# Kernel tuning notes

Hardware: AMD Instinct MI355X
Metric: run time of the kernel (lower is better)

Reference implementation:

```python
import jax, jax.numpy as jnp
import numpy as np


def setup_inputs() -> dict:
    key = jax.random.key(0)
    k1, k2 = jax.random.split(key)
    B, S, D, T = 64, 512, 768, 384
    hidden_states = jax.random.normal(k1, (B, S, D), dtype=jnp.float32)
    # sorted per-row segment ids: each subtoken belongs to a token index in [0, T)
    segment_ids = jnp.sort(jax.random.randint(k2, (B, S), 0, T), axis=-1)
    return {"hidden_states": hidden_states, "segment_ids": segment_ids, "num_tokens": T}


def reference(hidden_states, segment_ids, num_tokens):
    # Segment-mean of subtoken embeddings into token embeddings.
    # Equivalent to the original running-mean loop:
    #   prev + (next - prev) / n_subtoken_per_token  == mean over the group.
    B, S, D = hidden_states.shape
    # flatten batch into segment ids so one segment_sum handles all sequences
    flat_ids = (segment_ids + jnp.arange(B, dtype=segment_ids.dtype)[:, None] * num_tokens).reshape(-1)
    sums = jax.ops.segment_sum(hidden_states.reshape(-1, D), flat_ids,
                               num_segments=B * num_tokens)  # [B*T, D]
    counts = jax.ops.segment_sum(jnp.ones((B * S,), dtype=hidden_states.dtype), flat_ids,
                                 num_segments=B * num_tokens)  # [B*T]
    # tokens with no subtokens stay zero (original initializes with zeros)
    means = sums / jnp.maximum(counts, 1.0)[:, None]
    return means.reshape(B, num_tokens, D)
```

## Files before the change

kernel.cpp:

```cpp
#include <hip/hip_runtime.h>


#define PHASE2_WAVES 4

__global__ void bounds_pairs_kernel(const int* __restrict__ seg,
                                    const int* __restrict__ num_tokens_p,
                                    int2* __restrict__ pairs,
                                    int BS_total,
                                    int BT) {
  const int T = num_tokens_p[0];
  const int B = BT / T;
  const int S = BS_total / B;
  const int idx = blockIdx.x * blockDim.x + threadIdx.x;
  if (idx >= BS_total) return;
  const int b = idx / S;
  const int s = idx - b * S;
  const int cur = seg[idx];
  const int prev = (s == 0) ? -1 : seg[idx - 1];
  int2* __restrict__ prow = pairs + (size_t)b * T;

  for (int t = prev + 1; t <= cur; ++t) {
    prow[t].x = idx;
    if (t > 0) prow[t - 1].y = idx;
  }
  if (s == S - 1) {
    const int end = b * S + S;
    for (int t = cur + 1; t <= T; ++t) {
      if (t < T) prow[t].x = end;
      prow[t - 1].y = end;
    }
  }
}

__global__ void __launch_bounds__(64 * PHASE2_WAVES) seg_mean_d768(
    const float* __restrict__ hs,
    const int2*  __restrict__ pairs,
    float*       __restrict__ out,
    int BT) {
  const int wave = threadIdx.x >> 6;
  const int lane = threadIdx.x & 63;
  const int gstride = gridDim.x * PHASE2_WAVES;

  int g = blockIdx.x * PHASE2_WAVES + wave;
  if (g >= BT) return;
  int2 lh = pairs[g];

  while (true) {
    const int gn = g + gstride;
    int2 lh_next;
    if (gn < BT) lh_next = pairs[gn];

    const int cnt = lh.y - lh.x;
    const float4* __restrict__ p =
        (const float4*)hs + (size_t)lh.x * 192 + lane;

    float4 a0 = make_float4(0.f, 0.f, 0.f, 0.f);
    float4 a1 = a0, a2 = a0;
    for (int r = 0; r < cnt; ++r) {
      float4 v0 = p[0];
      float4 v1 = p[64];
      float4 v2 = p[128];
      a0.x += v0.x; a0.y += v0.y; a0.z += v0.z; a0.w += v0.w;
      a1.x += v1.x; a1.y += v1.y; a1.z += v1.z; a1.w += v1.w;
      a2.x += v2.x; a2.y += v2.y; a2.z += v2.z; a2.w += v2.w;
      p += 192;
    }

    const float inv = (cnt > 0) ? (1.0f / (float)cnt) : 0.0f;
    float4* __restrict__ q = (float4*)out + (size_t)g * 192 + lane;
    q[0]   = make_float4(a0.x * inv, a0.y * inv, a0.z * inv, a0.w * inv);
    q[64]  = make_float4(a1.x * inv, a1.y * inv, a1.z * inv, a1.w * inv);
    q[128] = make_float4(a2.x * inv, a2.y * inv, a2.z * inv, a2.w * inv);

    if (gn >= BT) break;
    g = gn;
    lh = lh_next;
  }
}

__global__ void __launch_bounds__(64 * PHASE2_WAVES) seg_mean_generic(
    const float* __restrict__ hs,
    const int2*  __restrict__ pairs,
    float*       __restrict__ out,
    int BT,
    int dv4) {
  const int wave = threadIdx.x >> 6;
  const int lane = threadIdx.x & 63;
  const int gstride = gridDim.x * PHASE2_WAVES;

  for (int g = blockIdx.x * PHASE2_WAVES + wave; g < BT; g += gstride) {
    const int2 lh = pairs[g];
    const int cnt = lh.y - lh.x;
    const float inv = (cnt > 0) ? (1.0f / (float)cnt) : 0.0f;

    for (int c = lane; c < dv4; c += 64) {
      const float4* __restrict__ p = (const float4*)hs + (size_t)lh.x * dv4 + c;
      float4 acc = make_float4(0.f, 0.f, 0.f, 0.f);
      for (int r = 0; r < cnt; ++r) {
        float4 v = *p;
        acc.x += v.x; acc.y += v.y; acc.z += v.z; acc.w += v.w;
        p += dv4;
      }
      ((float4*)(out + (size_t)g * (dv4 * 4)))[c] =
          make_float4(acc.x * inv, acc.y * inv, acc.z * inv, acc.w * inv);
    }
  }
}

__global__ void __launch_bounds__(192) seg_mean_search_kernel(
    const float* __restrict__ hs,
    const int* __restrict__ seg,
    const int* __restrict__ num_tokens_p,
    float* __restrict__ out,
    int BS_total,
    int D) {
  const int T = num_tokens_p[0];
  const int BT = gridDim.x;
  const int S = (int)(((long long)BS_total * T) / BT);
  const int b = blockIdx.x / T;
  const int t = blockIdx.x - b * T;
  const int* __restrict__ row = seg + (size_t)b * S;

  int lo = 0, n = S;
  while (n > 0) {
    int half = n >> 1;
    int mid = lo + half;
    if (row[mid] < t) { lo = mid + 1; n -= half + 1; } else { n = half; }
  }
  int hi = lo; n = S - lo;
  while (n > 0) {
    int half = n >> 1;
    int mid = hi + half;
    if (row[mid] < t + 1) { hi = mid + 1; n -= half + 1; } else { n = half; }
  }
  const int cnt = hi - lo;

  const int d4 = threadIdx.x;
  const int rowstride4 = D >> 2;
  const float4* __restrict__ p =
      (const float4*)(hs + ((size_t)b * S + lo) * D) + d4;

  float4 acc = make_float4(0.f, 0.f, 0.f, 0.f);
  for (int s = 0; s < cnt; ++s) {
    float4 v = p[(size_t)s * rowstride4];
    acc.x += v.x; acc.y += v.y; acc.z += v.z; acc.w += v.w;
  }
  const float inv = (cnt > 0) ? (1.0f / (float)cnt) : 0.0f;
  float4 o = make_float4(acc.x * inv, acc.y * inv, acc.z * inv, acc.w * inv);
  ((float4*)(out + (size_t)blockIdx.x * D))[d4] = o;
}

extern "C" void kernel_launch(void* const* d_in, const int* in_sizes, int n_in,
                              void* d_out, int out_size, void* d_ws, size_t ws_size,
                              hipStream_t stream) {
  const float* hs = (const float*)d_in[0];
  const int* seg = (const int*)d_in[1];
  const int* num_tokens_p = (const int*)d_in[2];
  float* out = (float*)d_out;

  const int BS_total = in_sizes[1];
  const int D = in_sizes[0] / in_sizes[1];
  const int BT = out_size / D;

  const size_t ws_needed = (size_t)8 * (size_t)BT;

  if (ws_size >= ws_needed) {
    int2* pairs = (int2*)d_ws;

    const int threads1 = 256;
    const int grid1 = (BS_total + threads1 - 1) / threads1;
    hipLaunchKernelGGL(bounds_pairs_kernel, dim3(grid1), dim3(threads1), 0, stream,
                       seg, num_tokens_p, pairs, BS_total, BT);

    const int maxBlocks = 2048;
    const int needBlocks = (BT + PHASE2_WAVES - 1) / PHASE2_WAVES;
    const int grid2 = (needBlocks < maxBlocks) ? needBlocks : maxBlocks;

    if (D == 768) {
      hipLaunchKernelGGL(seg_mean_d768, dim3(grid2), dim3(64 * PHASE2_WAVES), 0,
                         stream, hs, pairs, out, BT);
    } else {
      hipLaunchKernelGGL(seg_mean_generic, dim3(grid2), dim3(64 * PHASE2_WAVES), 0,
                         stream, hs, pairs, out, BT, D / 4);
    }
  } else {
    hipLaunchKernelGGL(seg_mean_search_kernel, dim3(BT), dim3(D / 4), 0, stream,
                       hs, seg, num_tokens_p, out, BS_total, D);
  }
}
```

Before: 178.0 us.

## Process spans of four tokens per wave with a 4-deep register load pipeline

The D=768 segment-mean kernel now gives each wave a contiguous span of four tokens and streams their subtoken rows through a software pipeline that keeps four rows of loads in flight in registers. Outputs are flushed each time a token boundary is crossed, and the grid is sized so there is no grid-stride loop. The aim is to hide memory latency, since each token has only about one or two rows and the old loop had few independent loads per wave. In exchange it uses more registers per thread, adds boundary-tracking branches, and launches more, smaller blocks.

```diff
diff --git a/kernel.cpp b/kernel.cpp
--- a/kernel.cpp
+++ b/kernel.cpp
@@ -1,7 +1,8 @@
 #include <hip/hip_runtime.h>
 
 
-#define PHASE2_WAVES 4
+#define SPAN_K 4
+#define WPB    4
 
 __global__ void bounds_pairs_kernel(const int* __restrict__ seg,
                                     const int* __restrict__ num_tokens_p,
@@ -32,53 +33,96 @@
   }
 }
 
-__global__ void __launch_bounds__(64 * PHASE2_WAVES) seg_mean_d768(
+__global__ void __launch_bounds__(64 * WPB, 4) seg_mean_span_d768(
     const float* __restrict__ hs,
     const int2*  __restrict__ pairs,
     float*       __restrict__ out,
     int BT) {
   const int wave = threadIdx.x >> 6;
   const int lane = threadIdx.x & 63;
-  const int gstride = gridDim.x * PHASE2_WAVES;
-
-  int g = blockIdx.x * PHASE2_WAVES + wave;
-  if (g >= BT) return;
-  int2 lh = pairs[g];
-
-  while (true) {
-    const int gn = g + gstride;
-    int2 lh_next;
-    if (gn < BT) lh_next = pairs[gn];
-
-    const int cnt = lh.y - lh.x;
-    const float4* __restrict__ p =
-        (const float4*)hs + (size_t)lh.x * 192 + lane;
-
-    float4 a0 = make_float4(0.f, 0.f, 0.f, 0.f);
-    float4 a1 = a0, a2 = a0;
-    for (int r = 0; r < cnt; ++r) {
-      float4 v0 = p[0];
-      float4 v1 = p[64];
-      float4 v2 = p[128];
-      a0.x += v0.x; a0.y += v0.y; a0.z += v0.z; a0.w += v0.w;
-      a1.x += v1.x; a1.y += v1.y; a1.z += v1.z; a1.w += v1.w;
-      a2.x += v2.x; a2.y += v2.y; a2.z += v2.z; a2.w += v2.w;
-      p += 192;
-    }
-
-    const float inv = (cnt > 0) ? (1.0f / (float)cnt) : 0.0f;
-    float4* __restrict__ q = (float4*)out + (size_t)g * 192 + lane;
-    q[0]   = make_float4(a0.x * inv, a0.y * inv, a0.z * inv, a0.w * inv);
-    q[64]  = make_float4(a1.x * inv, a1.y * inv, a1.z * inv, a1.w * inv);
-    q[128] = make_float4(a2.x * inv, a2.y * inv, a2.z * inv, a2.w * inv);
-
-    if (gn >= BT) break;
-    g = gn;
-    lh = lh_next;
-  }
-}
-
-__global__ void __launch_bounds__(64 * PHASE2_WAVES) seg_mean_generic(
+  const int g0 = (blockIdx.x * WPB + wave) * SPAN_K;
+  if (g0 >= BT) return;
+  const int nTok = (BT - g0 < SPAN_K) ? (BT - g0) : SPAN_K;
+
+  const int2 pL = pairs[g0 + nTok - 1];
+  const int sEnd = pL.y;
+  const int s0 = pairs[g0].x;
+  const int s1 = (nTok > 1) ? pairs[g0 + 1].x : sEnd;
+  const int s2 = (nTok > 2) ? pairs[g0 + 2].x : sEnd;
+  const int s3 = (nTok > 3) ? pairs[g0 + 3].x : sEnd;
+  const int s4 = sEnd;
+
+  const float4* __restrict__ hsv = (const float4*)hs;
+
+#define ISSUE(X0, X1, X2, ROW)                                   \
+  do {                                                           \
+    const float4* _p = hsv + (size_t)(ROW) * 192 + lane;         \
+    X0 = _p[0]; X1 = _p[64]; X2 = _p[128];                       \
+  } while (0)
+
+  float4 A0, A1, A2, B0, B1, B2, C0, C1, C2, D0, D1, D2;
+  int rowI = s0;
+  if (rowI < s4) { ISSUE(A0, A1, A2, rowI); ++rowI; }
+  if (rowI < s4) { ISSUE(B0, B1, B2, rowI); ++rowI; }
+  if (rowI < s4) { ISSUE(C0, C1, C2, rowI); ++rowI; }
+  if (rowI < s4) { ISSUE(D0, D1, D2, rowI); ++rowI; }
+
+  float4 acc0 = make_float4(0.f, 0.f, 0.f, 0.f);
+  float4 acc1 = acc0, acc2 = acc0;
+  int rowC = s0;
+  int tok = 0;
+  int curLo = s0;
+  int nb1 = s1, nb2 = s2, nb3 = s3;
+
+#define FLUSH()                                                               \
+  while (tok < nTok && rowC == nb1) {                                         \
+    const int _cnt = rowC - curLo;                                            \
+    const float _inv = (_cnt > 0) ? (1.0f / (float)_cnt) : 0.0f;              \
+    float4* _q = (float4*)out + (size_t)(g0 + tok) * 192 + lane;              \
+    _q[0]   = make_float4(acc0.x * _inv, acc0.y * _inv, acc0.z * _inv, acc0.w * _inv); \
+    _q[64]  = make_float4(acc1.x * _inv, acc1.y * _inv, acc1.z * _inv, acc1.w * _inv); \
+    _q[128] = make_float4(acc2.x * _inv, acc2.y * _inv, acc2.z * _inv, acc2.w * _inv); \
+    acc0 = make_float4(0.f, 0.f, 0.f, 0.f); acc1 = acc0; acc2 = acc0;         \
+    curLo = rowC; ++tok;                                                      \
+    nb1 = nb2; nb2 = nb3; nb3 = s4;                                           \
+  }
+
+#define CONSUME(X0, X1, X2)                                                   \
+  do {                                                                        \
+    acc0.x += X0.x; acc0.y += X0.y; acc0.z += X0.z; acc0.w += X0.w;           \
+    acc1.x += X1.x; acc1.y += X1.y; acc1.z += X1.z; acc1.w += X1.w;           \
+    acc2.x += X2.x; acc2.y += X2.y; acc2.z += X2.z; acc2.w += X2.w;           \
+    ++rowC;                                                                   \
+  } while (0)
+
+  FLUSH();
+  while (rowC < s4) {
+    CONSUME(A0, A1, A2);
+    if (rowI < s4) { ISSUE(A0, A1, A2, rowI); ++rowI; }
+    FLUSH();
+    if (rowC >= s4) break;
+
+    CONSUME(B0, B1, B2);
+    if (rowI < s4) { ISSUE(B0, B1, B2, rowI); ++rowI; }
+    FLUSH();
+    if (rowC >= s4) break;
+
+    CONSUME(C0, C1, C2);
+    if (rowI < s4) { ISSUE(C0, C1, C2, rowI); ++rowI; }
+    FLUSH();
+    if (rowC >= s4) break;
+
+    CONSUME(D0, D1, D2);
+    if (rowI < s4) { ISSUE(D0, D1, D2, rowI); ++rowI; }
+    FLUSH();
+  }
+
+#undef CONSUME
+#undef FLUSH
+#undef ISSUE
+}
+
+__global__ void __launch_bounds__(256) seg_mean_generic(
     const float* __restrict__ hs,
     const int2*  __restrict__ pairs,
     float*       __restrict__ out,
@@ -86,9 +130,9 @@
     int dv4) {
   const int wave = threadIdx.x >> 6;
   const int lane = threadIdx.x & 63;
-  const int gstride = gridDim.x * PHASE2_WAVES;
-
-  for (int g = blockIdx.x * PHASE2_WAVES + wave; g < BT; g += gstride) {
+  const int gstride = gridDim.x * 4;
+
+  for (int g = blockIdx.x * 4 + wave; g < BT; g += gstride) {
     const int2 lh = pairs[g];
     const int cnt = lh.y - lh.x;
     const float inv = (cnt > 0) ? (1.0f / (float)cnt) : 0.0f;
@@ -172,15 +216,15 @@
     hipLaunchKernelGGL(bounds_pairs_kernel, dim3(grid1), dim3(threads1), 0, stream,
                        seg, num_tokens_p, pairs, BS_total, BT);
 
-    const int maxBlocks = 2048;
-    const int needBlocks = (BT + PHASE2_WAVES - 1) / PHASE2_WAVES;
-    const int grid2 = (needBlocks < maxBlocks) ? needBlocks : maxBlocks;
-
     if (D == 768) {
-      hipLaunchKernelGGL(seg_mean_d768, dim3(grid2), dim3(64 * PHASE2_WAVES), 0,
+      const int tokensPerBlock = SPAN_K * WPB;
+      const int grid2 = (BT + tokensPerBlock - 1) / tokensPerBlock;
+      hipLaunchKernelGGL(seg_mean_span_d768, dim3(grid2), dim3(64 * WPB), 0,
                          stream, hs, pairs, out, BT);
     } else {
-      hipLaunchKernelGGL(seg_mean_generic, dim3(grid2), dim3(64 * PHASE2_WAVES), 0,
+      const int needBlocks = (BT + 3) / 4;
+      const int grid2 = (needBlocks < 2048) ? needBlocks : 2048;
+      hipLaunchKernelGGL(seg_mean_generic, dim3(grid2), dim3(256), 0,
                          stream, hs, pairs, out, BT, D / 4);
     }
   } else {
```

New measurement: 177.7 us. About the same (-0.1%).

## Use one 192-thread block per token with count specializations and nontemporal stores

Applied to the files above, without the earlier changes.

The D=768 path now launches one 192-thread block per output token instead of a grid-stride loop of one wave per token, so each thread handles one float4 column. Counts of 0, 1 and 2 get dedicated branches, and larger counts use a loop unrolled by two. Outputs are written with nontemporal stores to reduce cache pollution. This raises parallelism and memory-level concurrency at the cost of more blocks (24576) and dropping the prefetch of the next token's bounds.

```diff
diff --git a/kernel.cpp b/kernel.cpp
--- a/kernel.cpp
+++ b/kernel.cpp
@@ -1,7 +1,7 @@
 #include <hip/hip_runtime.h>
 
 
-#define PHASE2_WAVES 4
+typedef float f32x4_v __attribute__((ext_vector_type(4)));
 
 __global__ void bounds_pairs_kernel(const int* __restrict__ seg,
                                     const int* __restrict__ num_tokens_p,
@@ -32,53 +32,52 @@
   }
 }
 
-__global__ void __launch_bounds__(64 * PHASE2_WAVES) seg_mean_d768(
+__global__ void __launch_bounds__(192) seg_mean_tok_d768(
     const float* __restrict__ hs,
     const int2*  __restrict__ pairs,
-    float*       __restrict__ out,
-    int BT) {
-  const int wave = threadIdx.x >> 6;
-  const int lane = threadIdx.x & 63;
-  const int gstride = gridDim.x * PHASE2_WAVES;
+    float*       __restrict__ out) {
+  const int g = blockIdx.x;
+  const int2 lh = pairs[g];
+  const int cnt = lh.y - lh.x;
+  const int d4 = threadIdx.x;
 
-  int g = blockIdx.x * PHASE2_WAVES + wave;
-  if (g >= BT) return;
-  int2 lh = pairs[g];
+  const float4* __restrict__ p =
+      (const float4*)hs + (size_t)lh.x * 192 + d4;
+  f32x4_v* __restrict__ q = (f32x4_v*)out + (size_t)g * 192 + d4;
 
-  while (true) {
-    const int gn = g + gstride;
-    int2 lh_next;
-    if (gn < BT) lh_next = pairs[gn];
+  float4 o;
+  if (cnt == 1) {
+    o = p[0];
+  } else if (cnt == 0) {
+    o = make_float4(0.f, 0.f, 0.f, 0.f);
+  } else if (cnt == 2) {
+    float4 a = p[0];
+    float4 b = p[192];
+    o = make_float4((a.x + b.x) * 0.5f, (a.y + b.y) * 0.5f,
+                    (a.z + b.z) * 0.5f, (a.w + b.w) * 0.5f);
+  } else {
+    float4 acc = make_float4(0.f, 0.f, 0.f, 0.f);
+    int r = 0;
+    for (; r + 1 < cnt; r += 2) {
+      float4 a = p[(size_t)r * 192];
+      float4 b = p[(size_t)(r + 1) * 192];
+      acc.x += a.x + b.x; acc.y += a.y + b.y;
+      acc.z += a.z + b.z; acc.w += a.w + b.w;
+    }
+    if (r < cnt) {
+      float4 a = p[(size_t)r * 192];
+      acc.x += a.x; acc.y += a.y; acc.z += a.z; acc.w += a.w;
+    }
+    const float inv = 1.0f / (float)cnt;
+    o = make_float4(acc.x * inv, acc.y * inv, acc.z * inv, acc.w * inv);
+  }
 
-    const int cnt = lh.y - lh.x;
-    const float4* __restrict__ p =
-        (const float4*)hs + (size_t)lh.x * 192 + lane;
-
-    float4 a0 = make_float4(0.f, 0.f, 0.f, 0.f);
-    float4 a1 = a0, a2 = a0;
-    for (int r = 0; r < cnt; ++r) {
-      float4 v0 = p[0];
-      float4 v1 = p[64];
-      float4 v2 = p[128];
-      a0.x += v0.x; a0.y += v0.y; a0.z += v0.z; a0.w += v0.w;
-      a1.x += v1.x; a1.y += v1.y; a1.z += v1.z; a1.w += v1.w;
-      a2.x += v2.x; a2.y += v2.y; a2.z += v2.z; a2.w += v2.w;
-      p += 192;
-    }
-
-    const float inv = (cnt > 0) ? (1.0f / (float)cnt) : 0.0f;
-    float4* __restrict__ q = (float4*)out + (size_t)g * 192 + lane;
-    q[0]   = make_float4(a0.x * inv, a0.y * inv, a0.z * inv, a0.w * inv);
-    q[64]  = make_float4(a1.x * inv, a1.y * inv, a1.z * inv, a1.w * inv);
-    q[128] = make_float4(a2.x * inv, a2.y * inv, a2.z * inv, a2.w * inv);
-
-    if (gn >= BT) break;
-    g = gn;
-    lh = lh_next;
-  }
+  f32x4_v ov;
+  ov.x = o.x; ov.y = o.y; ov.z = o.z; ov.w = o.w;
+  __builtin_nontemporal_store(ov, q);
 }
 
-__global__ void __launch_bounds__(64 * PHASE2_WAVES) seg_mean_generic(
+__global__ void __launch_bounds__(256) seg_mean_generic(
     const float* __restrict__ hs,
     const int2*  __restrict__ pairs,
     float*       __restrict__ out,
@@ -86,9 +85,9 @@
     int dv4) {
   const int wave = threadIdx.x >> 6;
   const int lane = threadIdx.x & 63;
-  const int gstride = gridDim.x * PHASE2_WAVES;
+  const int gstride = gridDim.x * 4;
 
-  for (int g = blockIdx.x * PHASE2_WAVES + wave; g < BT; g += gstride) {
+  for (int g = blockIdx.x * 4 + wave; g < BT; g += gstride) {
     const int2 lh = pairs[g];
     const int cnt = lh.y - lh.x;
     const float inv = (cnt > 0) ? (1.0f / (float)cnt) : 0.0f;
@@ -172,15 +171,13 @@
     hipLaunchKernelGGL(bounds_pairs_kernel, dim3(grid1), dim3(threads1), 0, stream,
                        seg, num_tokens_p, pairs, BS_total, BT);
 
-    const int maxBlocks = 2048;
-    const int needBlocks = (BT + PHASE2_WAVES - 1) / PHASE2_WAVES;
-    const int grid2 = (needBlocks < maxBlocks) ? needBlocks : maxBlocks;
-
     if (D == 768) {
-      hipLaunchKernelGGL(seg_mean_d768, dim3(grid2), dim3(64 * PHASE2_WAVES), 0,
-                         stream, hs, pairs, out, BT);
+      hipLaunchKernelGGL(seg_mean_tok_d768, dim3(BT), dim3(192), 0, stream,
+                         hs, pairs, out);
     } else {
-      hipLaunchKernelGGL(seg_mean_generic, dim3(grid2), dim3(64 * PHASE2_WAVES), 0,
+      const int needBlocks = (BT + 3) / 4;
+      const int grid2 = (needBlocks < 2048) ? needBlocks : 2048;
+      hipLaunchKernelGGL(seg_mean_generic, dim3(grid2), dim3(256), 0,
                          stream, hs, pairs, out, BT, D / 4);
     }
   } else {
```

Measured after the change: 172.7 us. 1.03x faster.

## Split D768 segment mean into row-chunk blocks plus per-token fixup blocks

Applied to the files above, without the earlier changes.

Replaces the per-token grid-stride kernel with a hybrid launch. Chunk blocks each load 16 consecutive rows and emit means for segments that lie entirely inside the chunk. Fixup blocks, one wave per token, handle segments that cross a chunk boundary and empty tokens. The aim is to spread input reads evenly across many blocks with high memory-level parallelism, and outputs are written with nontemporal stores. The cost is a more complex boundary-detection scheme and a larger launch that now depends on the bounds workspace and the raw segment ids together.

```diff
diff --git a/kernel.cpp b/kernel.cpp
--- a/kernel.cpp
+++ b/kernel.cpp
@@ -1,7 +1,10 @@
 #include <hip/hip_runtime.h>
 
 
-#define PHASE2_WAVES 4
+typedef float f32x4_v __attribute__((ext_vector_type(4)));
+
+#define CHUNK 16
+#define CHUNK_SHIFT 4
 
 __global__ void bounds_pairs_kernel(const int* __restrict__ seg,
                                     const int* __restrict__ num_tokens_p,
@@ -32,28 +35,81 @@
   }
 }
 
-__global__ void __launch_bounds__(64 * PHASE2_WAVES) seg_mean_d768(
+__global__ void __launch_bounds__(192) seg_mean_chunk_d768(
     const float* __restrict__ hs,
+    const int*   __restrict__ seg,
     const int2*  __restrict__ pairs,
+    const int*   __restrict__ num_tokens_p,
     float*       __restrict__ out,
-    int BT) {
-  const int wave = threadIdx.x >> 6;
-  const int lane = threadIdx.x & 63;
-  const int gstride = gridDim.x * PHASE2_WAVES;
-
-  int g = blockIdx.x * PHASE2_WAVES + wave;
-  if (g >= BT) return;
-  int2 lh = pairs[g];
-
-  while (true) {
-    const int gn = g + gstride;
-    int2 lh_next;
-    if (gn < BT) lh_next = pairs[gn];
-
+    int BS_total,
+    int BT,
+    int nChunks) {
+  const int T = num_tokens_p[0];
+  const int B = BT / T;
+  const int S = BS_total / B;
+
+  if ((int)blockIdx.x < nChunks) {
+    const int r0 = blockIdx.x * CHUNK;
+    const int d4 = threadIdx.x;
+    const int rows = (BS_total - r0 < CHUNK) ? (BS_total - r0) : CHUNK;
+
+    const float4* __restrict__ hsv = (const float4*)hs;
+    float4 rv[CHUNK];
+#pragma unroll
+    for (int i = 0; i < CHUNK; ++i) {
+      if (i < rows) rv[i] = hsv[(size_t)(r0 + i) * 192 + d4];
+      else          rv[i] = make_float4(0.f, 0.f, 0.f, 0.f);
+    }
+
+    int sv[CHUNK + 2];
+    {
+      int bb = r0 / S;
+      int rib = r0 - bb * S;
+      sv[0] = (r0 == 0) ? -1
+            : (((rib == 0) ? (bb - 1) : bb) * T + seg[r0 - 1]);
+      int bi = bb, ri = rib;
+#pragma unroll
+      for (int i = 0; i < CHUNK; ++i) {
+        if (ri >= S) { ri -= S; ++bi; }
+        sv[i + 1] = (i < rows) ? (bi * T + seg[r0 + i]) : -1;
+        ++ri;
+      }
+      if (ri >= S) { ri -= S; ++bi; }
+      sv[CHUNK + 1] = (rows == CHUNK && r0 + CHUNK < BS_total)
+                        ? (bi * T + seg[r0 + CHUNK]) : -1;
+    }
+
+    float4 acc = make_float4(0.f, 0.f, 0.f, 0.f);
+    int runStart = 0;
+#pragma unroll
+    for (int i = 0; i < CHUNK; ++i) {
+      const float4 v = rv[i];
+      acc.x += v.x; acc.y += v.y; acc.z += v.z; acc.w += v.w;
+      if (sv[i + 2] != sv[i + 1]) {
+        if (sv[i + 1] >= 0 && (runStart > 0 || sv[0] != sv[1])) {
+          const int cnt = i - runStart + 1;
+          const float inv = 1.0f / (float)cnt;
+          f32x4_v o;
+          o.x = acc.x * inv; o.y = acc.y * inv;
+          o.z = acc.z * inv; o.w = acc.w * inv;
+          __builtin_nontemporal_store(
+              o, (f32x4_v*)out + (size_t)sv[i + 1] * 192 + d4);
+        }
+        acc = make_float4(0.f, 0.f, 0.f, 0.f);
+        runStart = i + 1;
+      }
+    }
+  } else {
+    const int g = ((int)blockIdx.x - nChunks) * 3 + (threadIdx.x >> 6);
+    if (g >= BT) return;
+    const int2 lh = pairs[g];
     const int cnt = lh.y - lh.x;
+    if (cnt > 0 && ((lh.x >> CHUNK_SHIFT) == ((lh.y - 1) >> CHUNK_SHIFT)))
+      return;
+
+    const int lane = threadIdx.x & 63;
     const float4* __restrict__ p =
         (const float4*)hs + (size_t)lh.x * 192 + lane;
-
     float4 a0 = make_float4(0.f, 0.f, 0.f, 0.f);
     float4 a1 = a0, a2 = a0;
     for (int r = 0; r < cnt; ++r) {
@@ -65,20 +121,19 @@
       a2.x += v2.x; a2.y += v2.y; a2.z += v2.z; a2.w += v2.w;
       p += 192;
     }
-
     const float inv = (cnt > 0) ? (1.0f / (float)cnt) : 0.0f;
-    float4* __restrict__ q = (float4*)out + (size_t)g * 192 + lane;
-    q[0]   = make_float4(a0.x * inv, a0.y * inv, a0.z * inv, a0.w * inv);
-    q[64]  = make_float4(a1.x * inv, a1.y * inv, a1.z * inv, a1.w * inv);
-    q[128] = make_float4(a2.x * inv, a2.y * inv, a2.z * inv, a2.w * inv);
-
-    if (gn >= BT) break;
-    g = gn;
-    lh = lh_next;
-  }
-}
-
-__global__ void __launch_bounds__(64 * PHASE2_WAVES) seg_mean_generic(
+    f32x4_v* __restrict__ q = (f32x4_v*)out + (size_t)g * 192 + lane;
+    f32x4_v o0, o1, o2;
+    o0.x = a0.x * inv; o0.y = a0.y * inv; o0.z = a0.z * inv; o0.w = a0.w * inv;
+    o1.x = a1.x * inv; o1.y = a1.y * inv; o1.z = a1.z * inv; o1.w = a1.w * inv;
+    o2.x = a2.x * inv; o2.y = a2.y * inv; o2.z = a2.z * inv; o2.w = a2.w * inv;
+    __builtin_nontemporal_store(o0, q);
+    __builtin_nontemporal_store(o1, q + 64);
+    __builtin_nontemporal_store(o2, q + 128);
+  }
+}
+
+__global__ void __launch_bounds__(256) seg_mean_generic(
     const float* __restrict__ hs,
     const int2*  __restrict__ pairs,
     float*       __restrict__ out,
@@ -86,9 +141,9 @@
     int dv4) {
   const int wave = threadIdx.x >> 6;
   const int lane = threadIdx.x & 63;
-  const int gstride = gridDim.x * PHASE2_WAVES;
-
-  for (int g = blockIdx.x * PHASE2_WAVES + wave; g < BT; g += gstride) {
+  const int gstride = gridDim.x * 4;
+
+  for (int g = blockIdx.x * 4 + wave; g < BT; g += gstride) {
     const int2 lh = pairs[g];
     const int cnt = lh.y - lh.x;
     const float inv = (cnt > 0) ? (1.0f / (float)cnt) : 0.0f;
@@ -172,15 +227,16 @@
     hipLaunchKernelGGL(bounds_pairs_kernel, dim3(grid1), dim3(threads1), 0, stream,
                        seg, num_tokens_p, pairs, BS_total, BT);
 
-    const int maxBlocks = 2048;
-    const int needBlocks = (BT + PHASE2_WAVES - 1) / PHASE2_WAVES;
-    const int grid2 = (needBlocks < maxBlocks) ? needBlocks : maxBlocks;
-
     if (D == 768) {
-      hipLaunchKernelGGL(seg_mean_d768, dim3(grid2), dim3(64 * PHASE2_WAVES), 0,
-                         stream, hs, pairs, out, BT);
+      const int nChunks = (BS_total + CHUNK - 1) / CHUNK;
+      const int nFix = (BT + 2) / 3;
+      hipLaunchKernelGGL(seg_mean_chunk_d768, dim3(nChunks + nFix), dim3(192),
+                         0, stream, hs, seg, pairs, num_tokens_p, out,
+                         BS_total, BT, nChunks);
     } else {
-      hipLaunchKernelGGL(seg_mean_generic, dim3(grid2), dim3(64 * PHASE2_WAVES), 0,
+      const int needBlocks = (BT + 3) / 4;
+      const int grid2 = (needBlocks < 2048) ? needBlocks : 2048;
+      hipLaunchKernelGGL(seg_mean_generic, dim3(grid2), dim3(256), 0,
                          stream, hs, pairs, out, BT, D / 4);
     }
   } else {
```

New measurement: 177.5 us. Within noise of the previous version (-0.2%).
